# Kernel optimization log

Measured on AMD Instinct MI355X. Metric: run time of the kernel, lower is better.

## Reference

```python
import jax, jax.numpy as jnp
import numpy as np

NEGPOS_RATIO = 3


def _smooth_l1(pred, tgt):
    d = jnp.abs(pred - tgt)
    return jnp.where(d < 1.0, 0.5 * d * d, d - 0.5)


def setup_inputs() -> dict:
    key = jax.random.key(0)
    B, P, C = 64, 8732, 81
    ks = jax.random.split(key, 7)
    loc_dataT = jax.random.normal(ks[0], (B, P, 4), jnp.float32)
    conf_dataT = jax.random.normal(ks[1], (B, P, C), jnp.float32)
    loc_dataS = jax.random.normal(ks[2], (B, P, 4), jnp.float32)
    conf_dataS = jax.random.normal(ks[3], (B, P, C), jnp.float32)
    loc_t = jax.random.normal(ks[4], (B, P, 4), jnp.float32)
    is_pos = jax.random.uniform(ks[5], (B, P)) < 0.02
    labels = jax.random.randint(ks[6], (B, P), 1, C, dtype=jnp.int32)
    conf_t = jnp.where(is_pos, labels, 0).astype(jnp.int32)
    return {
        "loc_dataT": loc_dataT, "conf_dataT": conf_dataT,
        "loc_dataS": loc_dataS, "conf_dataS": conf_dataS,
        "loc_t": loc_t, "conf_t": conf_t,
    }


def _multibox_losses(loc_dataT, conf_dataT, loc_dataS, conf_dataS, loc_t, conf_t):
    B, P, C = conf_dataT.shape
    pos = conf_t > 0                                    # [B,P]
    posf = pos.astype(conf_dataT.dtype)

    # Localization SmoothL1 over positive priors (reduction='sum')
    loss_lT = jnp.sum(_smooth_l1(loc_dataT, loc_t) * posf[..., None])
    loss_lS = jnp.sum(_smooth_l1(loc_dataS, loc_t) * posf[..., None])

    # Per-prior CE loss: logsumexp(conf) - conf[gt]  (== -log_softmax[gt])
    def per_prior_ce(conf):
        lse = jax.nn.logsumexp(conf, axis=-1)           # [B,P]
        gt = jnp.take_along_axis(conf, conf_t[..., None].astype(jnp.int32), axis=-1)[..., 0]
        return lse - gt

    lcT = per_prior_ce(conf_dataT)                      # [B,P]
    lcS = per_prior_ce(conf_dataS)

    # Hard negative mining: rank negatives by loss (positives zeroed first)
    def neg_mask(lc, num_neg):
        lc_m = jnp.where(pos, 0.0, lc)
        order = jnp.argsort(-lc_m, axis=1)              # descending sort indices
        rank = jnp.argsort(order, axis=1)               # rank of each prior
        return rank < num_neg

    num_pos = jnp.sum(pos.astype(jnp.int32), axis=1, keepdims=True)   # [B,1]
    num_neg = jnp.minimum(NEGPOS_RATIO * num_pos, P - 1)
    negT = neg_mask(lcT, num_neg)
    negS = neg_mask(lcS, num_neg)

    # Confidence CE over positives + mined negatives (reduction='sum')
    loss_cT = jnp.sum(jnp.where(pos | negT, lcT, 0.0))
    loss_cS = jnp.sum(jnp.where(pos | negS, lcS, 0.0))

    N = jnp.sum(num_pos).astype(conf_dataT.dtype)
    return jnp.stack([loss_lT / N, loss_cT / N, loss_lS / N, loss_cS / N])


def reference(loc_dataT, conf_dataT, loc_dataS, conf_dataS, loc_t, conf_t):
    # Teacher branch is detached in the original module.
    loc_dataT = jax.lax.stop_gradient(loc_dataT)
    conf_dataT = jax.lax.stop_gradient(conf_dataT)
    return _multibox_losses(loc_dataT, conf_dataT, loc_dataS, conf_dataS, loc_t, conf_t)
```

## Files before the change

### kernel.cpp

```cpp
#include <hip/hip_runtime.h>
#include <hip/hip_bf16.h>

#define BB 64
#define PP 8732
#define CC 81
#define RPB 128


__device__ __forceinline__ float sl1(float d) {
    d = fabsf(d);
    return d < 1.0f ? 0.5f * d * d : d - 0.5f;
}

__device__ __forceinline__ float blockReduceF(float v, volatile float* sb) {
    for (int off = 32; off; off >>= 1) v += __shfl_xor(v, off, 64);
    __syncthreads();
    if ((threadIdx.x & 63) == 0) sb[threadIdx.x >> 6] = v;
    __syncthreads();
    float r = 0.0f;
    int nw = blockDim.x >> 6;
    for (int i = 0; i < nw; ++i) r += sb[i];
    return r;
}

__device__ __forceinline__ int blockReduceI(int v, volatile int* sb) {
    for (int off = 32; off; off >>= 1) v += __shfl_xor(v, off, 64);
    __syncthreads();
    if ((threadIdx.x & 63) == 0) sb[threadIdx.x >> 6] = v;
    __syncthreads();
    int r = 0;
    int nw = blockDim.x >> 6;
    for (int i = 0; i < nw; ++i) r += sb[i];
    return r;
}

__global__ void kInit(float* acc, int* numpos) {
    int t = threadIdx.x;
    if (t < 4) acc[t] = 0.0f;
    if (t < BB) numpos[t] = 0;
}

__global__ __launch_bounds__(1024) void kA(const float4* __restrict__ locT,
                                           const float4* __restrict__ locS,
                                           const float4* __restrict__ loct,
                                           const int* __restrict__ conft,
                                           float* acc, int* numpos) {
    __shared__ float fsb[16];
    __shared__ int isb[16];
    int b = blockIdx.y;
    int p = blockIdx.x * blockDim.x + threadIdx.x;
    float sT = 0.0f, sS = 0.0f;
    int cnt = 0;
    if (p < PP) {
        size_t i = (size_t)b * PP + p;
        int t = conft[i];
        if (t > 0) {
            cnt = 1;
            float4 g = loct[i];
            float4 aT = locT[i];
            float4 aS = locS[i];
            sT = sl1(aT.x - g.x) + sl1(aT.y - g.y) + sl1(aT.z - g.z) + sl1(aT.w - g.w);
            sS = sl1(aS.x - g.x) + sl1(aS.y - g.y) + sl1(aS.z - g.z) + sl1(aS.w - g.w);
        }
    }
    sT = blockReduceF(sT, fsb);
    sS = blockReduceF(sS, fsb);
    cnt = blockReduceI(cnt, isb);
    if (threadIdx.x == 0) {
        if (sT != 0.0f) atomicAdd(&acc[0], sT);
        if (sS != 0.0f) atomicAdd(&acc[1], sS);
        if (cnt) atomicAdd(&numpos[b], cnt);
    }
}

__global__ __launch_bounds__(512) void kB(const float* __restrict__ confT,
                                          const float* __restrict__ confS,
                                          const int* __restrict__ conft,
                                          float* __restrict__ lcT,
                                          float* __restrict__ lcS) {
    __shared__ float tile[RPB * CC + 4];
    int b = blockIdx.y;
    int p0 = blockIdx.x * RPB;
    int nrows = min(RPB, PP - p0);
    int nq = (nrows * CC) >> 2;
    int tid = threadIdx.x;
    int r = tid >> 2, sub = tid & 3;
    int limit = (sub == 3) ? 18 : 21;
    size_t rowBase = (size_t)b * PP + p0;
    int gt = (r < nrows) ? conft[rowBase + r] : 0;

    const float* __restrict__ srcs[2] = {confT, confS};
    float* __restrict__ dsts[2] = {lcT, lcS};

    for (int x = 0; x < 2; ++x) {
        const float4* g4 = (const float4*)(srcs[x] + rowBase * CC);
        for (int i = tid; i < nq; i += 512) ((float4*)tile)[i] = g4[i];
        __syncthreads();
        if (r < nrows) {
            const float* rowp = tile + r * CC + sub * 21;
            float s = 0.0f;
            #pragma unroll
            for (int i = 0; i < 21; ++i) {
                float e = __expf(rowp[i]);
                s += (i < limit) ? e : 0.0f;
            }
            s += __shfl_xor(s, 1, 64);
            s += __shfl_xor(s, 2, 64);
            float lc = __logf(s) - tile[r * CC + gt];
            if (sub == 0) dsts[x][rowBase + r] = (gt > 0) ? -(lc + 1.0f) : lc;
        }
        __syncthreads();
    }
}

__global__ __launch_bounds__(1024) void kC(const float* __restrict__ lcT,
                                           const float* __restrict__ lcS,
                                           const int* __restrict__ numpos,
                                           float* acc) {
    __shared__ unsigned keys[PP];
    __shared__ int hist[256];
    __shared__ float fsb[16];
    __shared__ int isb[16];
    __shared__ int selBin, selAbove;
    int b = blockIdx.y;
    int tid = threadIdx.x;
    const float* src = ((blockIdx.x == 0) ? lcT : lcS) + (size_t)b * PP;

    float posSum = 0.0f;
    for (int i = tid; i < PP; i += 1024) {
        float v = src[i];
        keys[i] = (v < 0.0f) ? 0u : __float_as_uint(v);
        if (v < 0.0f) posSum += (-v - 1.0f);
    }
    posSum = blockReduceF(posSum, fsb);

    int np = numpos[b];
    int k = min(3 * np, PP - 1);
    float mined = 0.0f;
    if (k > 0) {
        unsigned prefix = 0;
        int kk = k;
        for (int round = 0; round < 4; ++round) {
            int shift = 24 - 8 * round;
            if (tid < 256) hist[tid] = 0;
            __syncthreads();
            for (int i = tid; i < PP; i += 1024) {
                unsigned key = keys[i];
                bool match = (round == 0) || ((key >> (shift + 8)) == prefix);
                if (match) atomicAdd(&hist[(key >> shift) & 0xFF], 1);
            }
            __syncthreads();
            for (int d = 1; d < 256; d <<= 1) {
                int v2 = 0;
                if (tid < 256) v2 = hist[tid] + ((tid + d < 256) ? hist[tid + d] : 0);
                __syncthreads();
                if (tid < 256) hist[tid] = v2;
                __syncthreads();
            }
            if (tid < 256) {
                int above = (tid < 255) ? hist[tid + 1] : 0;
                if (above < kk && hist[tid] >= kk) {
                    selBin = tid;
                    selAbove = above;
                }
            }
            __syncthreads();
            prefix = (prefix << 8) | (unsigned)selBin;
            kk -= selAbove;
            __syncthreads();
        }
        int c = 0;
        float s = 0.0f;
        for (int i = tid; i < PP; i += 1024) {
            unsigned key = keys[i];
            if (key > prefix) { c += 1; s += __uint_as_float(key); }
        }
        c = blockReduceI(c, isb);
        s = blockReduceF(s, fsb);
        mined = s + (float)(k - c) * __uint_as_float(prefix);
    }
    if (tid == 0) atomicAdd(&acc[(blockIdx.x == 0) ? 2 : 3], posSum + mined);
}

__global__ void kD(const float* acc, const int* numpos, float* out) {
    int v = (threadIdx.x < BB) ? numpos[threadIdx.x] : 0;
    for (int off = 32; off; off >>= 1) v += __shfl_xor(v, off, 64);
    if (threadIdx.x == 0) {
        float N = (float)v;
        out[0] = acc[0] / N;
        out[1] = acc[2] / N;
        out[2] = acc[1] / N;
        out[3] = acc[3] / N;
    }
}

extern "C" void kernel_launch(void* const* d_in, const int* in_sizes, int n_in,
                              void* d_out, int out_size, void* d_ws, size_t ws_size,
                              hipStream_t stream) {
    const float* locT  = (const float*)d_in[0];
    const float* confT = (const float*)d_in[1];
    const float* locS  = (const float*)d_in[2];
    const float* confS = (const float*)d_in[3];
    const float* loct  = (const float*)d_in[4];
    const int*   conft = (const int*)d_in[5];
    float* out = (float*)d_out;

    float* lcT = (float*)d_ws;
    float* lcS = lcT + (size_t)BB * PP;
    float* acc = lcS + (size_t)BB * PP;
    int* numpos = (int*)(acc + 4);

    kInit<<<1, 64, 0, stream>>>(acc, numpos);

    dim3 gA((PP + 1023) / 1024, BB);
    kA<<<gA, 1024, 0, stream>>>((const float4*)locT, (const float4*)locS,
                                (const float4*)loct, conft, acc, numpos);

    dim3 gB((PP + RPB - 1) / RPB, BB);
    kB<<<gB, 512, 0, stream>>>(confT, confS, conft, lcT, lcS);

    dim3 gC(2, BB);
    kC<<<gC, 1024, 0, stream>>>(lcT, lcS, numpos, acc);

    kD<<<1, 64, 0, stream>>>(acc, numpos, out);
}
```

Baseline: 425.9 us.

## Stream conf logits directly with LDS atomic row sums instead of tiling

The CE kernel no longer stages a 128x81 tile in shared memory. Each thread now reads a float4 from global memory, exponentiates it, and adds the partial sums into per-row shared-memory accumulators with atomics. It also captures the ground-truth logit on the fly. Teacher and student move to a separate grid z dimension with 256-thread blocks. This cuts LDS footprint and raises occupancy, so more loads can be in flight for this bandwidth-bound pass. The cost is integer division by 81 per element and contention on the shared-memory atomics.

```diff
diff --git a/kernel.cpp b/kernel.cpp
--- a/kernel.cpp
+++ b/kernel.cpp
@@ -73,43 +73,62 @@
     }
 }
 
-__global__ __launch_bounds__(512) void kB(const float* __restrict__ confT,
+__global__ __launch_bounds__(256) void kB(const float* __restrict__ confT,
                                           const float* __restrict__ confS,
                                           const int* __restrict__ conft,
                                           float* __restrict__ lcT,
                                           float* __restrict__ lcS) {
-    __shared__ float tile[RPB * CC + 4];
+    __shared__ float rowsum[RPB];
+    __shared__ float gtval[RPB];
+    __shared__ int gtofs[RPB];
+    __shared__ int gtraw[RPB];
     int b = blockIdx.y;
     int p0 = blockIdx.x * RPB;
     int nrows = min(RPB, PP - p0);
+    int tid = threadIdx.x;
+    const float* __restrict__ conf = blockIdx.z ? confS : confT;
+    float* __restrict__ dst = blockIdx.z ? lcS : lcT;
+    size_t rowBase = (size_t)b * PP + p0;
+
+    for (int r = tid; r < nrows; r += 256) {
+        int g = conft[rowBase + r];
+        gtraw[r] = g;
+        gtofs[r] = r * CC + g;
+        rowsum[r] = 0.0f;
+        gtval[r] = 0.0f;
+    }
+    __syncthreads();
+
+    const float4* __restrict__ g4 = (const float4*)(conf + rowBase * CC);
     int nq = (nrows * CC) >> 2;
-    int tid = threadIdx.x;
-    int r = tid >> 2, sub = tid & 3;
-    int limit = (sub == 3) ? 18 : 21;
-    size_t rowBase = (size_t)b * PP + p0;
-    int gt = (r < nrows) ? conft[rowBase + r] : 0;
-
-    const float* __restrict__ srcs[2] = {confT, confS};
-    float* __restrict__ dsts[2] = {lcT, lcS};
-
-    for (int x = 0; x < 2; ++x) {
-        const float4* g4 = (const float4*)(srcs[x] + rowBase * CC);
-        for (int i = tid; i < nq; i += 512) ((float4*)tile)[i] = g4[i];
-        __syncthreads();
-        if (r < nrows) {
-            const float* rowp = tile + r * CC + sub * 21;
-            float s = 0.0f;
-            #pragma unroll
-            for (int i = 0; i < 21; ++i) {
-                float e = __expf(rowp[i]);
-                s += (i < limit) ? e : 0.0f;
-            }
-            s += __shfl_xor(s, 1, 64);
-            s += __shfl_xor(s, 2, 64);
-            float lc = __logf(s) - tile[r * CC + gt];
-            if (sub == 0) dsts[x][rowBase + r] = (gt > 0) ? -(lc + 1.0f) : lc;
-        }
-        __syncthreads();
+    for (int i = tid; i < nq; i += 256) {
+        float4 v = g4[i];
+        int f = i << 2;
+        int r0 = f / 81;
+        int rem = f - r0 * 81;
+        int r1 = (rem + 3 >= 81) ? r0 + 1 : r0;
+        float e0 = __expf(v.x), e1 = __expf(v.y), e2 = __expf(v.z), e3 = __expf(v.w);
+        float t01 = e0 + e1, t23 = e2 + e3, tot = t01 + t23;
+        if (r1 == r0) {
+            atomicAdd(&rowsum[r0], tot);
+        } else {
+            int nsplit = 81 - rem;
+            float a = (nsplit == 1) ? e0 : ((nsplit == 2) ? t01 : t01 + e2);
+            atomicAdd(&rowsum[r0], a);
+            atomicAdd(&rowsum[r1], tot - a);
+        }
+        int j = gtofs[r0] - f;
+        if (j >= 0 && j < 4) gtval[r0] = ((const float*)&v)[j];
+        if (r1 != r0) {
+            int j1 = gtofs[r1] - f;
+            if (j1 >= 0 && j1 < 4) gtval[r1] = ((const float*)&v)[j1];
+        }
+    }
+    __syncthreads();
+
+    for (int r = tid; r < nrows; r += 256) {
+        float lc = __logf(rowsum[r]) - gtval[r];
+        dst[rowBase + r] = (gtraw[r] > 0) ? -(lc + 1.0f) : lc;
     }
 }
 
@@ -216,8 +235,8 @@
     kA<<<gA, 1024, 0, stream>>>((const float4*)locT, (const float4*)locS,
                                 (const float4*)loct, conft, acc, numpos);
 
-    dim3 gB((PP + RPB - 1) / RPB, BB);
-    kB<<<gB, 512, 0, stream>>>(confT, confS, conft, lcT, lcS);
+    dim3 gB((PP + RPB - 1) / RPB, BB, 2);
+    kB<<<gB, 256, 0, stream>>>(confT, confS, conft, lcT, lcS);
 
     dim3 gC(2, BB);
     kC<<<gC, 1024, 0, stream>>>(lcT, lcS, numpos, acc);
```

After: 509.2 us. +19.6%, slower.
